# Kernel tuning notes

Hardware: AMD Instinct MI355X
Metric: run time of the kernel (lower is better)

Reference implementation:

```python
import jax, jax.numpy as jnp
import numpy as np

B, C, H, W = 4, 256, 64, 64
C8 = C // 8


def _xavier(key, shape):
    fan_in, fan_out = shape[1], shape[0]
    limit = float(np.sqrt(6.0 / (fan_in + fan_out)))
    return jax.random.uniform(key, shape, jnp.float32, -limit, limit)


def setup_inputs() -> dict:
    key = jax.random.key(0)
    ks = jax.random.split(key, 10)
    inp = {
        "x": jax.random.normal(ks[0], (B, C, H, W), jnp.float32),
        "y": jax.random.normal(ks[1], (B, C, H, W), jnp.float32),
        "Wfx": _xavier(ks[2], (C8, C)), "bfx": jnp.zeros((C8,), jnp.float32),
        "Wgx": _xavier(ks[3], (C8, C)), "bgx": jnp.zeros((C8,), jnp.float32),
        "Whx": _xavier(ks[4], (C, C)),  "bhx": jnp.zeros((C,), jnp.float32),
        "Wfy": _xavier(ks[5], (C8, C)), "bfy": jnp.zeros((C8,), jnp.float32),
        "Wgy": _xavier(ks[6], (C8, C)), "bgy": jnp.zeros((C8,), jnp.float32),
        "Why": _xavier(ks[7], (C, C)),  "bhy": jnp.zeros((C,), jnp.float32),
        # torch init is gamma=0 which zeroes the attention branch; use a random
        # scalar so the reference exercises the full computation.
        "gamma": jax.random.normal(ks[8], (1,), jnp.float32),
    }
    return inp


def _conv1x1(x, Wt, b):
    # 1x1 conv == per-pixel linear over channels; output flattened to [B, O, N]
    b_, c, h, w = x.shape
    out = jnp.einsum('oc,bchw->bohw', Wt, x) + b[None, :, None, None]
    return out.reshape(b_, -1, h * w)


def reference(x, y, Wfx, bfx, Wgx, bgx, Whx, bhx, Wfy, bfy, Wgy, bgy, Why, bhy, gamma):
    b, c, h, w = x.shape
    fx = _conv1x1(x, Wfx, bfx)  # [B, C8, N]
    gx = _conv1x1(x, Wgx, bgx)
    hx = _conv1x1(x, Whx, bhx)  # [B, C, N]
    fy = _conv1x1(y, Wfy, bfy)
    gy = _conv1x1(y, Wgy, bgy)
    hy = _conv1x1(y, Why, bhy)

    # attention_x = softmax(f_y^T @ g_x) over last dim; [B, N, N]
    att_x = jax.nn.softmax(jnp.einsum('bcn,bcm->bnm', fy, gx), axis=-1)
    att_y = jax.nn.softmax(jnp.einsum('bcn,bcm->bnm', fx, gy), axis=-1)

    sa_x = jnp.einsum('bcn,bnm->bcm', hx, att_x).reshape(b, c, h, w)
    sa_y = jnp.einsum('bcn,bnm->bcm', hy, att_y).reshape(b, c, h, w)

    out_x = gamma[0] * sa_x + x
    out_y = gamma[0] * sa_y + y
    return (out_x, out_y)
```

## Files before the change

kernel.cpp:

```cpp
#include <hip/hip_runtime.h>

#define BB 4
#define CC 256
#define NN 4096

typedef _Float16 half_t;
typedef __attribute__((ext_vector_type(8))) _Float16 half8;
typedef __attribute__((ext_vector_type(4))) _Float16 half4;
typedef __attribute__((ext_vector_type(4))) float floatx4;
typedef __attribute__((ext_vector_type(16))) float floatx16;

__global__ __launch_bounds__(256)
void cvt_w_kernel(const float* __restrict__ Wfx, const float* __restrict__ Wgx,
                  const float* __restrict__ Whx, const float* __restrict__ Wfy,
                  const float* __restrict__ Wgy, const float* __restrict__ Why,
                  half_t* __restrict__ oWfx, half_t* __restrict__ oWgx,
                  half_t* __restrict__ oWhx, half_t* __restrict__ oWfy,
                  half_t* __restrict__ oWgy, half_t* __restrict__ oWhy)
{
    const float* src; half_t* dst; int n;
    switch (blockIdx.y) {
        case 0: src = Wfx; dst = oWfx; n = 32 * CC; break;
        case 1: src = Wgx; dst = oWgx; n = 32 * CC; break;
        case 2: src = Whx; dst = oWhx; n = CC * CC; break;
        case 3: src = Wfy; dst = oWfy; n = 32 * CC; break;
        case 4: src = Wgy; dst = oWgy; n = 32 * CC; break;
        default: src = Why; dst = oWhy; n = CC * CC; break;
    }
    int idx = (blockIdx.x * 256 + threadIdx.x) * 4;
    if (idx >= n) return;
    float4 v = *(const float4*)&src[idx];
    half4 h; h[0] = (half_t)v.x; h[1] = (half_t)v.y; h[2] = (half_t)v.z; h[3] = (half_t)v.w;
    *(half4*)&dst[idx] = h;
}

__global__ __launch_bounds__(256)
void transpose_cvt_kernel(const float* __restrict__ x, const float* __restrict__ y,
                          half_t* __restrict__ xTx, half_t* __restrict__ xTy)
{
    const int n0 = blockIdx.x * 64;
    const int c0 = blockIdx.y * 64;
    const int b  = blockIdx.z & 3;
    const int sel = blockIdx.z >> 2;
    const float* in = sel ? y : x;
    half_t* outT = sel ? xTy : xTx;
    const int t  = threadIdx.x;
    const int ch = t & 7, nl = t >> 3;
    const float* inb = in + (size_t)b * CC * NN;
    half_t* outb = outT + (size_t)b * NN * CC;

    #pragma unroll
    for (int p = 0; p < 2; ++p) {
        int n = n0 + nl + 32 * p;
        half8 hv;
        #pragma unroll
        for (int j = 0; j < 8; ++j)
            hv[j] = (half_t)inb[(size_t)(c0 + 8 * ch + j) * NN + n];
        *(half8*)&outb[(size_t)n * CC + c0 + 8 * ch] = hv;
    }
}

__global__ __launch_bounds__(256)
void proj_fg_kernel(const half_t* __restrict__ xTx, const half_t* __restrict__ xTy,
                    const half_t* __restrict__ Wfx, const half_t* __restrict__ Wgx,
                    const half_t* __restrict__ Wfy, const half_t* __restrict__ Wgy,
                    const float* __restrict__ bfx, const float* __restrict__ bgx,
                    const float* __restrict__ bfy, const float* __restrict__ bgy,
                    half_t* __restrict__ fxT, half_t* __restrict__ gxT,
                    half_t* __restrict__ fyT, half_t* __restrict__ gyT)
{
    const int n0 = blockIdx.x * 64;
    const int b  = blockIdx.y;
    const int sel = blockIdx.z;
    const half_t* xT = sel ? xTy : xTx;
    const half_t* Wf = sel ? Wfy : Wfx;
    const half_t* Wg = sel ? Wgy : Wgx;
    const float*  bf = sel ? bfy : bfx;
    const float*  bg = sel ? bgy : bgx;
    half_t* fT = sel ? fyT : fxT;
    half_t* gT = sel ? gyT : gxT;

    const int t  = threadIdx.x;
    const int w = t >> 6, lane = t & 63, q = lane >> 4, mc = lane & 15;
    const half_t* xTb = xT + (size_t)b * NN * CC;

    floatx4 acc[4];
    #pragma unroll
    for (int i = 0; i < 4; ++i) {
        float bv = (i < 2 ? bf : bg)[(i & 1) * 16 + mc];
        acc[i] = (floatx4){bv, bv, bv, bv};
    }

    #pragma unroll
    for (int ks = 0; ks < 8; ++ks) {
        int k0 = ks * 32 + q * 8;
        half8 af = *(const half8*)&xTb[(size_t)(n0 + w * 16 + mc) * CC + k0];
        #pragma unroll
        for (int i = 0; i < 4; ++i) {
            const half_t* Ws = (i < 2) ? Wf : Wg;
            half8 bfr = *(const half8*)&Ws[(size_t)((i & 1) * 16 + mc) * CC + k0];
            acc[i] = __builtin_amdgcn_mfma_f32_16x16x32_f16(af, bfr, acc[i], 0, 0, 0);
        }
    }

    #pragma unroll
    for (int i = 0; i < 4; ++i) {
        half_t* dst = (i < 2) ? fT : gT;
        #pragma unroll
        for (int r = 0; r < 4; ++r) {
            int n = n0 + w * 16 + q * 4 + r;
            dst[((size_t)b * NN + n) * 32 + (i & 1) * 16 + mc] = (half_t)acc[i][r];
        }
    }
}

__global__ __launch_bounds__(256)
void proj_h_kernel(const half_t* __restrict__ xTx, const half_t* __restrict__ xTy,
                   const half_t* __restrict__ Whx, const half_t* __restrict__ Why,
                   const float* __restrict__ bhx, const float* __restrict__ bhy,
                   half_t* __restrict__ hx, half_t* __restrict__ hy)
{
    const int n0 = blockIdx.x * 64;
    const int o0 = blockIdx.y * 128;
    const int b  = blockIdx.z & 3;
    const int sel = blockIdx.z >> 2;
    const half_t* xT = sel ? xTy : xTx;
    const half_t* Wh = sel ? Why : Whx;
    const float*  bh = sel ? bhy : bhx;
    half_t* h = sel ? hy : hx;

    const int t  = threadIdx.x;
    const int w = t >> 6, lane = t & 63, q = lane >> 4, mc = lane & 15;
    const half_t* xTb = xT + (size_t)b * NN * CC;
    half_t* hb = h + (size_t)b * CC * NN;

    floatx4 acc[2][4];
    #pragma unroll
    for (int j = 0; j < 2; ++j) {
        floatx4 bv;
        #pragma unroll
        for (int r = 0; r < 4; ++r) bv[r] = bh[o0 + w * 32 + j * 16 + q * 4 + r];
        #pragma unroll
        for (int i = 0; i < 4; ++i) acc[j][i] = bv;
    }

    #pragma unroll
    for (int ks = 0; ks < 8; ++ks) {
        int k0 = ks * 32 + q * 8;
        half8 a0 = *(const half8*)&Wh[(size_t)(o0 + w * 32 + mc) * CC + k0];
        half8 a1 = *(const half8*)&Wh[(size_t)(o0 + w * 32 + 16 + mc) * CC + k0];
        #pragma unroll
        for (int i = 0; i < 4; ++i) {
            half8 bfr = *(const half8*)&xTb[(size_t)(n0 + i * 16 + mc) * CC + k0];
            acc[0][i] = __builtin_amdgcn_mfma_f32_16x16x32_f16(a0, bfr, acc[0][i], 0, 0, 0);
            acc[1][i] = __builtin_amdgcn_mfma_f32_16x16x32_f16(a1, bfr, acc[1][i], 0, 0, 0);
        }
    }

    #pragma unroll
    for (int j = 0; j < 2; ++j)
        #pragma unroll
        for (int i = 0; i < 4; ++i)
            #pragma unroll
            for (int r = 0; r < 4; ++r) {
                int o = o0 + w * 32 + j * 16 + q * 4 + r;
                hb[(size_t)o * NN + n0 + i * 16 + mc] = (half_t)acc[j][i][r];
            }
}

__global__ __launch_bounds__(256)
void stats_kernel(const half_t* __restrict__ fT0, const half_t* __restrict__ gT0,
                  const half_t* __restrict__ fT1, const half_t* __restrict__ gT1,
                  float* __restrict__ L0, float* __restrict__ L1)
{
    __shared__ float red_l[4][32];
    const int b  = blockIdx.y;
    const int sel = blockIdx.z;
    const half_t* fT = sel ? fT1 : fT0;
    const half_t* gT = sel ? gT1 : gT0;
    float* Lout = sel ? L1 : L0;

    const int n0 = blockIdx.x * 32;
    const int t  = threadIdx.x;
    const int w = t >> 6, lane = t & 63, q = lane >> 4, mc = lane & 15;
    const half_t* fTb = fT + (size_t)b * NN * 32;
    const half_t* gTb = gT + (size_t)b * NN * 32;

    half8 a0 = *(const half8*)&fTb[(size_t)(n0 + mc) * 32 + q * 8];
    half8 a1 = *(const half8*)&fTb[(size_t)(n0 + 16 + mc) * 32 + q * 8];

    float l0[4] = {0.f, 0.f, 0.f, 0.f}, l1[4] = {0.f, 0.f, 0.f, 0.f};
    for (int it = 0; it < NN / 64; ++it) {
        int m = (it * 4 + w) * 16 + mc;
        half8 bfr = *(const half8*)&gTb[(size_t)m * 32 + q * 8];
        floatx4 S0 = __builtin_amdgcn_mfma_f32_16x16x32_f16(a0, bfr, (floatx4){0.f,0.f,0.f,0.f}, 0, 0, 0);
        floatx4 S1 = __builtin_amdgcn_mfma_f32_16x16x32_f16(a1, bfr, (floatx4){0.f,0.f,0.f,0.f}, 0, 0, 0);
        #pragma unroll
        for (int r = 0; r < 4; ++r) { l0[r] += __expf(S0[r]); l1[r] += __expf(S1[r]); }
    }
    #pragma unroll
    for (int r = 0; r < 4; ++r) {
        #pragma unroll
        for (int off = 1; off < 16; off <<= 1) {
            l0[r] += __shfl_xor(l0[r], off);
            l1[r] += __shfl_xor(l1[r], off);
        }
    }
    if (mc == 0)
        #pragma unroll
        for (int r = 0; r < 4; ++r) {
            red_l[w][q * 4 + r]      = l0[r];
            red_l[w][16 + q * 4 + r] = l1[r];
        }
    __syncthreads();
    if (t < 32) {
        float L = red_l[0][t] + red_l[1][t] + red_l[2][t] + red_l[3][t];
        Lout[(size_t)b * NN + n0 + t] = -log2f(L);
    }
}

__global__ __launch_bounds__(512, 4)
void pv_kernel(const half_t* __restrict__ fT0, const half_t* __restrict__ gT0,
               const half_t* __restrict__ h0, const float* __restrict__ L0,
               const float* __restrict__ src0, float* __restrict__ out0,
               const half_t* __restrict__ fT1, const half_t* __restrict__ gT1,
               const half_t* __restrict__ h1, const float* __restrict__ L1,
               const float* __restrict__ src1, float* __restrict__ out1,
               const float* __restrict__ gamma)
{
    __shared__ half_t h_lds[256][72];
    __shared__ half_t PT[64][72];

    const int m0 = blockIdx.x * 64;
    const int b  = blockIdx.y & 3;
    const int sel = blockIdx.y >> 2;
    const half_t* fT = sel ? fT1 : fT0;
    const half_t* gT = sel ? gT1 : gT0;
    const half_t* h  = sel ? h1 : h0;
    const float*  Lg = sel ? L1 : L0;
    const float*  src = sel ? src1 : src0;
    float* out = sel ? out1 : out0;

    const int t = threadIdx.x;
    const int w = t >> 6, lane = t & 63;
    const int q = lane >> 4, mc = lane & 15;
    const int l5 = lane >> 5, l31 = lane & 31;

    const int mg  = (w >> 1) * 16;
    const int nhf = (w & 1) * 32;

    const half_t* fTb = fT + (size_t)b * NN * 32;
    const half_t* gTb = gT + (size_t)b * NN * 32;
    const half_t* hb  = h + (size_t)b * CC * NN;
    const float*  Lb  = Lg + (size_t)b * NN;

    const half8 gS = *(const half8*)&gTb[(size_t)(m0 + mg + mc) * 32 + q * 8];

    const int srow = t >> 3;
    const int sch  = t & 7;

    half8 hpre[4]; half8 fpre[2]; float4 lv[2];
    #pragma unroll
    for (int i = 0; i < 4; ++i)
        hpre[i] = *(const half8*)&hb[(size_t)(srow + 64 * i) * NN + sch * 8];
    #pragma unroll
    for (int s = 0; s < 2; ++s) {
        fpre[s] = *(const half8*)&fTb[(size_t)(nhf + s * 16 + mc) * 32 + q * 8];
        lv[s]   = *(const float4*)&Lb[nhf + s * 16 + q * 4];
    }

    floatx16 acc[2];
    #pragma unroll
    for (int bm = 0; bm < 2; ++bm)
        #pragma unroll
        for (int r = 0; r < 16; ++r) acc[bm][r] = 0.f;

    for (int nt = 0; nt < NN; nt += 64) {
        __syncthreads();
        #pragma unroll
        for (int i = 0; i < 4; ++i)
            *(half8*)&h_lds[srow + 64 * i][sch * 8] = hpre[i];

        #pragma unroll
        for (int s = 0; s < 2; ++s) {
            floatx4 S = __builtin_amdgcn_mfma_f32_16x16x32_f16(
                fpre[s], gS, (floatx4){0.f, 0.f, 0.f, 0.f}, 0, 0, 0);
            half4 p;
            p[0] = (half_t)exp2f(fmaf(S[0], 1.44269504f, lv[s].x));
            p[1] = (half_t)exp2f(fmaf(S[1], 1.44269504f, lv[s].y));
            p[2] = (half_t)exp2f(fmaf(S[2], 1.44269504f, lv[s].z));
            p[3] = (half_t)exp2f(fmaf(S[3], 1.44269504f, lv[s].w));
            *(half4*)&PT[mg + mc][nhf + s * 16 + q * 4] = p;
        }
        __syncthreads();

        int ntn = nt + 64; if (ntn >= NN) ntn = 0;
        #pragma unroll
        for (int i = 0; i < 4; ++i)
            hpre[i] = *(const half8*)&hb[(size_t)(srow + 64 * i) * NN + ntn + sch * 8];
        #pragma unroll
        for (int s = 0; s < 2; ++s) {
            fpre[s] = *(const half8*)&fTb[(size_t)(ntn + nhf + s * 16 + mc) * 32 + q * 8];
            lv[s]   = *(const float4*)&Lb[ntn + nhf + s * 16 + q * 4];
        }

        #pragma unroll
        for (int ch = 0; ch < 4; ++ch) {
            half8 Ah = *(const half8*)&h_lds[w * 32 + l31][ch * 16 + l5 * 8];
            half8 B0 = *(const half8*)&PT[l31][ch * 16 + l5 * 8];
            half8 B1 = *(const half8*)&PT[32 + l31][ch * 16 + l5 * 8];
            acc[0] = __builtin_amdgcn_mfma_f32_32x32x16_f16(Ah, B0, acc[0], 0, 0, 0);
            acc[1] = __builtin_amdgcn_mfma_f32_32x32x16_f16(Ah, B1, acc[1], 0, 0, 0);
        }
    }

    const float gm = gamma[0];
    const float* srcb = src + (size_t)b * CC * NN;
    float* outb = out + (size_t)b * CC * NN;
    #pragma unroll
    for (int bm = 0; bm < 2; ++bm) {
        const int m = m0 + bm * 32 + l31;
        #pragma unroll
        for (int r = 0; r < 16; ++r) {
            int c = w * 32 + (r & 3) + 8 * (r >> 2) + 4 * l5;
            size_t idx = (size_t)c * NN + m;
            outb[idx] = fmaf(gm, acc[bm][r], srcb[idx]);
        }
    }
}

extern "C" void kernel_launch(void* const* d_in, const int* in_sizes, int n_in,
                              void* d_out, int out_size, void* d_ws, size_t ws_size,
                              hipStream_t stream)
{
    const float* x   = (const float*)d_in[0];
    const float* y   = (const float*)d_in[1];
    const float* Wfx = (const float*)d_in[2];
    const float* bfx = (const float*)d_in[3];
    const float* Wgx = (const float*)d_in[4];
    const float* bgx = (const float*)d_in[5];
    const float* Whx = (const float*)d_in[6];
    const float* bhx = (const float*)d_in[7];
    const float* Wfy = (const float*)d_in[8];
    const float* bfy = (const float*)d_in[9];
    const float* Wgy = (const float*)d_in[10];
    const float* bgy = (const float*)d_in[11];
    const float* Why = (const float*)d_in[12];
    const float* bhy = (const float*)d_in[13];
    const float* gam = (const float*)d_in[14];

    const size_t SZ_XT = (size_t)BB * NN * CC;
    const size_t SZ_FG = (size_t)BB * NN * 32;
    half_t* xTx   = (half_t*)d_ws;
    half_t* xTy   = xTx + SZ_XT;
    half_t* hx    = xTy + SZ_XT;
    half_t* hy    = hx + SZ_XT;
    half_t* fxT   = hy + SZ_XT;
    half_t* gxT   = fxT + SZ_FG;
    half_t* fyT   = gxT + SZ_FG;
    half_t* gyT   = fyT + SZ_FG;
    half_t* Wfx_h = gyT + SZ_FG;
    half_t* Wgx_h = Wfx_h + 32 * CC;
    half_t* Wfy_h = Wgx_h + 32 * CC;
    half_t* Wgy_h = Wfy_h + 32 * CC;
    half_t* Whx_h = Wgy_h + 32 * CC;
    half_t* Why_h = Whx_h + CC * CC;
    float*  Lx    = (float*)(Why_h + CC * CC);
    float*  Ly    = Lx + (size_t)BB * NN;

    float* outx = (float*)d_out;
    float* outy = outx + (size_t)BB * CC * NN;

    cvt_w_kernel<<<dim3(64, 6), 256, 0, stream>>>(Wfx, Wgx, Whx, Wfy, Wgy, Why,
                                                  Wfx_h, Wgx_h, Whx_h, Wfy_h, Wgy_h, Why_h);

    transpose_cvt_kernel<<<dim3(64, 4, 8), 256, 0, stream>>>(x, y, xTx, xTy);

    proj_fg_kernel<<<dim3(64, 4, 2), 256, 0, stream>>>(
        xTx, xTy, Wfx_h, Wgx_h, Wfy_h, Wgy_h, bfx, bgx, bfy, bgy, fxT, gxT, fyT, gyT);

    proj_h_kernel<<<dim3(64, 2, 8), 256, 0, stream>>>(
        xTx, xTy, Whx_h, Why_h, bhx, bhy, hx, hy);

    stats_kernel<<<dim3(128, 4, 2), 256, 0, stream>>>(fyT, gxT, fxT, gyT, Lx, Ly);

    pv_kernel<<<dim3(64, 8), 512, 0, stream>>>(
        fyT, gxT, hx, Lx, x, outx,
        fxT, gyT, hy, Ly, y, outy, gam);
}
```

Baseline: 281.4 us.

## Double-buffer P tile and compute next softmax tile during PV MFMAs

The PV kernel now double-buffers the probability tile in shared memory. The exp/softmax for tile T+1 is computed and written to the alternate buffer while MFMAs consume tile T. This removes one sync-separated phase per iteration, so the transcendental work can overlap with matrix cores. It also raises wave priority around the MFMA block. The cost is extra LDS (about 9KB more), extra registers for prefetched f/L two tiles ahead, and a prologue computing the first tile.

```diff
diff --git a/kernel.cpp b/kernel.cpp
--- a/kernel.cpp
+++ b/kernel.cpp
@@ -229,7 +229,7 @@
                const float* __restrict__ gamma)
 {
     __shared__ half_t h_lds[256][72];
-    __shared__ half_t PT[64][72];
+    __shared__ half_t PT[2][64][72];
 
     const int m0 = blockIdx.x * 64;
     const int b  = blockIdx.y & 3;
@@ -259,59 +259,94 @@
     const int srow = t >> 3;
     const int sch  = t & 7;
 
-    half8 hpre[4]; half8 fpre[2]; float4 lv[2];
+    const half_t* hP = hb + (size_t)srow * NN + sch * 8;
+    const half_t* fP = fTb + (size_t)(nhf + mc) * 32 + q * 8;
+    const float*  lP = Lb + nhf + q * 4;
+
+    floatx16 acc[2];
+    #pragma unroll
+    for (int bm = 0; bm < 2; ++bm)
+        #pragma unroll
+        for (int r = 0; r < 16; ++r) acc[bm][r] = 0.f;
+
+    half8 hpre[4];
+    half8 fu[2], ff[2];
+    floatx4 lvu[2], lvf[2];
+
+    {
+        half8 f0[2]; floatx4 l0[2];
+        #pragma unroll
+        for (int s = 0; s < 2; ++s) {
+            f0[s] = *(const half8*)&fP[(size_t)(s * 16) * 32];
+            l0[s] = *(const floatx4*)&lP[s * 16];
+        }
+        #pragma unroll
+        for (int s = 0; s < 2; ++s) {
+            floatx4 S = __builtin_amdgcn_mfma_f32_16x16x32_f16(
+                f0[s], gS, (floatx4){0.f, 0.f, 0.f, 0.f}, 0, 0, 0);
+            half4 p;
+            p[0] = (half_t)exp2f(fmaf(S[0], 1.44269504f, l0[s][0]));
+            p[1] = (half_t)exp2f(fmaf(S[1], 1.44269504f, l0[s][1]));
+            p[2] = (half_t)exp2f(fmaf(S[2], 1.44269504f, l0[s][2]));
+            p[3] = (half_t)exp2f(fmaf(S[3], 1.44269504f, l0[s][3]));
+            *(half4*)&PT[0][mg + mc][nhf + s * 16 + q * 4] = p;
+        }
+    }
     #pragma unroll
     for (int i = 0; i < 4; ++i)
-        hpre[i] = *(const half8*)&hb[(size_t)(srow + 64 * i) * NN + sch * 8];
+        hpre[i] = *(const half8*)&hP[(size_t)(64 * i) * NN];
     #pragma unroll
     for (int s = 0; s < 2; ++s) {
-        fpre[s] = *(const half8*)&fTb[(size_t)(nhf + s * 16 + mc) * 32 + q * 8];
-        lv[s]   = *(const float4*)&Lb[nhf + s * 16 + q * 4];
-    }
-
-    floatx16 acc[2];
-    #pragma unroll
-    for (int bm = 0; bm < 2; ++bm)
-        #pragma unroll
-        for (int r = 0; r < 16; ++r) acc[bm][r] = 0.f;
-
-    for (int nt = 0; nt < NN; nt += 64) {
+        fu[s]  = *(const half8*)&fP[(size_t)(64 + s * 16) * 32];
+        lvu[s] = *(const floatx4*)&lP[64 + s * 16];
+    }
+
+    #pragma unroll 2
+    for (int T = 0; T < NN / 64; ++T) {
+        const int cur = T & 1, nxt = cur ^ 1;
+
         __syncthreads();
         #pragma unroll
         for (int i = 0; i < 4; ++i)
             *(half8*)&h_lds[srow + 64 * i][sch * 8] = hpre[i];
+        __syncthreads();
+
+        int ntn  = (T + 1) * 64; if (ntn  >= NN) ntn  = 0;
+        int ntn2 = (T + 2) * 64; if (ntn2 >= NN) ntn2 -= NN;
+        #pragma unroll
+        for (int i = 0; i < 4; ++i)
+            hpre[i] = *(const half8*)&hP[(size_t)(64 * i) * NN + ntn];
+        #pragma unroll
+        for (int s = 0; s < 2; ++s) {
+            ff[s]  = *(const half8*)&fP[(size_t)(ntn2 + s * 16) * 32];
+            lvf[s] = *(const floatx4*)&lP[ntn2 + s * 16];
+        }
 
         #pragma unroll
         for (int s = 0; s < 2; ++s) {
             floatx4 S = __builtin_amdgcn_mfma_f32_16x16x32_f16(
-                fpre[s], gS, (floatx4){0.f, 0.f, 0.f, 0.f}, 0, 0, 0);
+                fu[s], gS, (floatx4){0.f, 0.f, 0.f, 0.f}, 0, 0, 0);
             half4 p;
-            p[0] = (half_t)exp2f(fmaf(S[0], 1.44269504f, lv[s].x));
-            p[1] = (half_t)exp2f(fmaf(S[1], 1.44269504f, lv[s].y));
-            p[2] = (half_t)exp2f(fmaf(S[2], 1.44269504f, lv[s].z));
-            p[3] = (half_t)exp2f(fmaf(S[3], 1.44269504f, lv[s].w));
-            *(half4*)&PT[mg + mc][nhf + s * 16 + q * 4] = p;
-        }
-        __syncthreads();
-
-        int ntn = nt + 64; if (ntn >= NN) ntn = 0;
-        #pragma unroll
-        for (int i = 0; i < 4; ++i)
-            hpre[i] = *(const half8*)&hb[(size_t)(srow + 64 * i) * NN + ntn + sch * 8];
-        #pragma unroll
-        for (int s = 0; s < 2; ++s) {
-            fpre[s] = *(const half8*)&fTb[(size_t)(ntn + nhf + s * 16 + mc) * 32 + q * 8];
-            lv[s]   = *(const float4*)&Lb[ntn + nhf + s * 16 + q * 4];
-        }
-
+            p[0] = (half_t)exp2f(fmaf(S[0], 1.44269504f, lvu[s][0]));
+            p[1] = (half_t)exp2f(fmaf(S[1], 1.44269504f, lvu[s][1]));
+            p[2] = (half_t)exp2f(fmaf(S[2], 1.44269504f, lvu[s][2]));
+            p[3] = (half_t)exp2f(fmaf(S[3], 1.44269504f, lvu[s][3]));
+            *(half4*)&PT[nxt][mg + mc][nhf + s * 16 + q * 4] = p;
+        }
+
+        __builtin_amdgcn_s_setprio(1);
         #pragma unroll
         for (int ch = 0; ch < 4; ++ch) {
             half8 Ah = *(const half8*)&h_lds[w * 32 + l31][ch * 16 + l5 * 8];
-            half8 B0 = *(const half8*)&PT[l31][ch * 16 + l5 * 8];
-            half8 B1 = *(const half8*)&PT[32 + l31][ch * 16 + l5 * 8];
+            half8 B0 = *(const half8*)&PT[cur][l31][ch * 16 + l5 * 8];
+            half8 B1 = *(const half8*)&PT[cur][32 + l31][ch * 16 + l5 * 8];
             acc[0] = __builtin_amdgcn_mfma_f32_32x32x16_f16(Ah, B0, acc[0], 0, 0, 0);
             acc[1] = __builtin_amdgcn_mfma_f32_32x32x16_f16(Ah, B1, acc[1], 0, 0, 0);
         }
+        __builtin_amdgcn_s_setprio(0);
+
+        #pragma unroll
+        for (int s = 0; s < 2; ++s) { fu[s] = ff[s]; lvu[s] = lvf[s]; }
     }
 
     const float gm = gamma[0];
```

Result: no change. 282.9 us (+0.5%).
